# Kernel tuning notes

Hardware: AMD Instinct MI355X
Metric: run time of the kernel (lower is better)

The kernel has to match this reference:

```python
import jax, jax.numpy as jnp
import numpy as np

REGION_MAX = 116
DEFAULT_REGION_ID = 0


def setup_inputs() -> dict:
    key = jax.random.key(0)
    k1, k2, k3, k4 = jax.random.split(key, 4)
    B, N = 16, 4096
    D, H, W = 182, 218, 182
    embed_dim = 768
    # patch centers in MRI voxel space; range slightly exceeds the atlas so
    # some points land out-of-bounds and exercise the default-region path.
    patch_centers_voxels = jax.random.uniform(k1, (B, N, 3), dtype=jnp.float32) * 230.0 - 20.0
    # use identity-like affines (typical co-registered case)
    mri_affine = jnp.eye(4, dtype=jnp.float32)
    aal_affine = jnp.eye(4, dtype=jnp.float32)
    # atlas volume with integer region labels stored as float (nib get_fdata)
    aal_data = jax.random.randint(k3, (D, H, W), 0, REGION_MAX + 1).astype(jnp.float32)
    embed_table = jax.random.normal(k4, (REGION_MAX + 1, embed_dim), dtype=jnp.float32)
    return {
        "patch_centers_voxels": patch_centers_voxels,
        "mri_affine": mri_affine,
        "aal_affine": aal_affine,
        "aal_data": aal_data,
        "embed_table": embed_table,
    }


def reference(patch_centers_voxels, mri_affine, aal_affine, aal_data, embed_table):
    B, N, _ = patch_centers_voxels.shape
    D, H, W = aal_data.shape
    # homogeneous voxel coords -> world coords -> atlas voxel coords
    ones = jnp.ones((B, N, 1), dtype=patch_centers_voxels.dtype)
    voxel_homo = jnp.concatenate([patch_centers_voxels, ones], axis=-1)  # [B,N,4]
    world = jnp.einsum('ij,bnj->bni', mri_affine, voxel_homo)
    inv_aal = jnp.linalg.inv(aal_affine)
    aal_vox = jnp.einsum('ij,bnj->bni', inv_aal, world)[..., :3]  # [B,N,3]
    idx = jnp.round(aal_vox).astype(jnp.int32)  # [B,N,3]
    x, y, z = idx[..., 0], idx[..., 1], idx[..., 2]
    in_bounds = (
        (x >= 0) & (x < D) & (y >= 0) & (y < H) & (z >= 0) & (z < W)
    )
    cx = jnp.clip(x, 0, D - 1)
    cy = jnp.clip(y, 0, H - 1)
    cz = jnp.clip(z, 0, W - 1)
    region = aal_data[cx, cy, cz].astype(jnp.int32)  # [B,N]
    valid = in_bounds & (region >= 0) & (region <= REGION_MAX)
    region_ids = jnp.where(valid, region, DEFAULT_REGION_ID)
    return embed_table[region_ids]  # [B,N,embed_dim]
```

## Files before the change

kernel.cpp:

```cpp
#include <hip/hip_runtime.h>
#include <math.h>

#define REGION_MAX 116
#define EMB 768
#define EMB4 192
#define DIM_D 182
#define DIM_H 218
#define DIM_W 182

typedef float v4f __attribute__((ext_vector_type(4)));

__global__ __launch_bounds__(256) void region_kernel(
    const float* __restrict__ centers,
    const float* __restrict__ mri,
    const float* __restrict__ aal,
    const float* __restrict__ vol,
    int* __restrict__ rid_out,
    int P) {
    __shared__ float M[12];
    if (threadIdx.x == 0) {
        float a[4][8];
        for (int i = 0; i < 4; ++i)
            for (int j = 0; j < 4; ++j) {
                a[i][j]     = aal[i * 4 + j];
                a[i][j + 4] = (i == j) ? 1.0f : 0.0f;
            }
        for (int c = 0; c < 4; ++c) {
            int piv = c;
            float best = fabsf(a[c][c]);
            for (int r = c + 1; r < 4; ++r) {
                float v = fabsf(a[r][c]);
                if (v > best) { best = v; piv = r; }
            }
            if (piv != c)
                for (int j = 0; j < 8; ++j) {
                    float t = a[c][j]; a[c][j] = a[piv][j]; a[piv][j] = t;
                }
            float inv = 1.0f / a[c][c];
            for (int j = 0; j < 8; ++j) a[c][j] *= inv;
            for (int r = 0; r < 4; ++r) {
                if (r == c) continue;
                float f = a[r][c];
                for (int j = 0; j < 8; ++j) a[r][j] -= f * a[c][j];
            }
        }
        for (int i = 0; i < 3; ++i)
            for (int j = 0; j < 4; ++j) {
                float s = 0.0f;
                for (int k = 0; k < 4; ++k) s += a[i][4 + k] * mri[k * 4 + j];
                M[i * 4 + j] = s;
            }
    }
    __syncthreads();

    int p = blockIdx.x * blockDim.x + threadIdx.x;
    if (p >= P) return;

    float px = centers[p * 3 + 0];
    float py = centers[p * 3 + 1];
    float pz = centers[p * 3 + 2];

    float fx = M[0] * px + M[1] * py + M[2]  * pz + M[3];
    float fy = M[4] * px + M[5] * py + M[6]  * pz + M[7];
    float fz = M[8] * px + M[9] * py + M[10] * pz + M[11];

    int x = (int)rintf(fx);
    int y = (int)rintf(fy);
    int z = (int)rintf(fz);

    bool inb = (x >= 0) & (x < DIM_D) & (y >= 0) & (y < DIM_H) &
               (z >= 0) & (z < DIM_W);
    int cx = min(max(x, 0), DIM_D - 1);
    int cy = min(max(y, 0), DIM_H - 1);
    int cz = min(max(z, 0), DIM_W - 1);

    int region = (int)vol[((size_t)cx * DIM_H + cy) * DIM_W + cz];
    rid_out[p] = (inb && region >= 0 && region <= REGION_MAX) ? region : 0;
}

__global__ __launch_bounds__(256) void copy_kernel(
    const int* __restrict__ rid,
    const float* __restrict__ table,
    float* __restrict__ out,
    long total4) {
    long i = (long)blockIdx.x * blockDim.x + threadIdx.x;
    if (i >= total4) return;
    long p = i / EMB4;
    int  c = (int)(i - p * EMB4);
    int  r = rid[p];
    const v4f* __restrict__ src = (const v4f*)(table) + (long)r * EMB4 + c;
    v4f v = *src;
    __builtin_nontemporal_store(v, ((v4f*)out) + i);
}

extern "C" void kernel_launch(void* const* d_in, const int* in_sizes, int n_in,
                              void* d_out, int out_size, void* d_ws, size_t ws_size,
                              hipStream_t stream) {
    const float* centers = (const float*)d_in[0];
    const float* mri     = (const float*)d_in[1];
    const float* aal     = (const float*)d_in[2];
    const float* vol     = (const float*)d_in[3];
    const float* table   = (const float*)d_in[4];
    float* out = (float*)d_out;
    int*   rid = (int*)d_ws;

    int P = in_sizes[0] / 3;

    int blocks1 = (P + 255) / 256;
    region_kernel<<<blocks1, 256, 0, stream>>>(centers, mri, aal, vol, rid, P);

    long total4 = (long)P * EMB4;
    int blocks2 = (int)((total4 + 255) / 256);
    copy_kernel<<<blocks2, 256, 0, stream>>>(rid, table, out, total4);
}
```

Baseline: 227.2 us.

## Fuse region lookup and embedding gather into one kernel with shared region ids

Merges the region-index kernel and the embedding copy kernel into a single kernel. Each block handles 32 points: the first 32 threads compute region ids into shared memory, then all 256 threads stream the corresponding table rows out with nontemporal stores. This removes one launch, the workspace round trip for region ids, and the per-element 64-bit division. In exchange every block redoes the 4x4 matrix inverse and issues two barriers, and the id-computation phase is serialized ahead of the copy.

```diff
diff --git a/kernel.cpp b/kernel.cpp
--- a/kernel.cpp
+++ b/kernel.cpp
@@ -7,17 +7,22 @@
 #define DIM_D 182
 #define DIM_H 218
 #define DIM_W 182
+#define PPB 32
+#define BLOCK 256
 
 typedef float v4f __attribute__((ext_vector_type(4)));
 
-__global__ __launch_bounds__(256) void region_kernel(
+__global__ __launch_bounds__(BLOCK) void fused_embed_kernel(
     const float* __restrict__ centers,
     const float* __restrict__ mri,
     const float* __restrict__ aal,
     const float* __restrict__ vol,
-    int* __restrict__ rid_out,
+    const float* __restrict__ table,
+    float* __restrict__ out,
     int P) {
     __shared__ float M[12];
+    __shared__ int rids[PPB];
+
     if (threadIdx.x == 0) {
         float a[4][8];
         for (int i = 0; i < 4; ++i)
@@ -53,44 +58,57 @@
     }
     __syncthreads();
 
-    int p = blockIdx.x * blockDim.x + threadIdx.x;
-    if (p >= P) return;
+    const int base = blockIdx.x * PPB;
 
-    float px = centers[p * 3 + 0];
-    float py = centers[p * 3 + 1];
-    float pz = centers[p * 3 + 2];
+    if (threadIdx.x < PPB) {
+        const int p = base + threadIdx.x;
+        int r = 0;
+        if (p < P) {
+            float px = centers[p * 3 + 0];
+            float py = centers[p * 3 + 1];
+            float pz = centers[p * 3 + 2];
 
-    float fx = M[0] * px + M[1] * py + M[2]  * pz + M[3];
-    float fy = M[4] * px + M[5] * py + M[6]  * pz + M[7];
-    float fz = M[8] * px + M[9] * py + M[10] * pz + M[11];
+            float fx = M[0] * px + M[1] * py + M[2]  * pz + M[3];
+            float fy = M[4] * px + M[5] * py + M[6]  * pz + M[7];
+            float fz = M[8] * px + M[9] * py + M[10] * pz + M[11];
 
-    int x = (int)rintf(fx);
-    int y = (int)rintf(fy);
-    int z = (int)rintf(fz);
+            int x = (int)rintf(fx);
+            int y = (int)rintf(fy);
+            int z = (int)rintf(fz);
 
-    bool inb = (x >= 0) & (x < DIM_D) & (y >= 0) & (y < DIM_H) &
-               (z >= 0) & (z < DIM_W);
-    int cx = min(max(x, 0), DIM_D - 1);
-    int cy = min(max(y, 0), DIM_H - 1);
-    int cz = min(max(z, 0), DIM_W - 1);
+            bool inb = (x >= 0) & (x < DIM_D) & (y >= 0) & (y < DIM_H) &
+                       (z >= 0) & (z < DIM_W);
+            int cx = min(max(x, 0), DIM_D - 1);
+            int cy = min(max(y, 0), DIM_H - 1);
+            int cz = min(max(z, 0), DIM_W - 1);
 
-    int region = (int)vol[((size_t)cx * DIM_H + cy) * DIM_W + cz];
-    rid_out[p] = (inb && region >= 0 && region <= REGION_MAX) ? region : 0;
-}
+            int region = (int)vol[((size_t)cx * DIM_H + cy) * DIM_W + cz];
+            r = (inb && region >= 0 && region <= REGION_MAX) ? region : 0;
+        }
+        rids[threadIdx.x] = r;
+    }
+    __syncthreads();
 
-__global__ __launch_bounds__(256) void copy_kernel(
-    const int* __restrict__ rid,
-    const float* __restrict__ table,
-    float* __restrict__ out,
-    long total4) {
-    long i = (long)blockIdx.x * blockDim.x + threadIdx.x;
-    if (i >= total4) return;
-    long p = i / EMB4;
-    int  c = (int)(i - p * EMB4);
-    int  r = rid[p];
-    const v4f* __restrict__ src = (const v4f*)(table) + (long)r * EMB4 + c;
-    v4f v = *src;
-    __builtin_nontemporal_store(v, ((v4f*)out) + i);
+    const int npts = min(PPB, P - base);
+    const v4f* __restrict__ tab4 = (const v4f*)table;
+    v4f* __restrict__ out4 = (v4f*)out + (long)base * EMB4;
+
+    if (npts == PPB) {
+        #pragma unroll 4
+        for (unsigned j = threadIdx.x; j < (unsigned)(PPB * EMB4); j += BLOCK) {
+            unsigned p = j / (unsigned)EMB4;
+            unsigned c = j - p * (unsigned)EMB4;
+            v4f v = tab4[(unsigned)rids[p] * EMB4 + c];
+            __builtin_nontemporal_store(v, out4 + j);
+        }
+    } else {
+        for (unsigned j = threadIdx.x; j < (unsigned)(npts * EMB4); j += BLOCK) {
+            unsigned p = j / (unsigned)EMB4;
+            unsigned c = j - p * (unsigned)EMB4;
+            v4f v = tab4[(unsigned)rids[p] * EMB4 + c];
+            __builtin_nontemporal_store(v, out4 + j);
+        }
+    }
 }
 
 extern "C" void kernel_launch(void* const* d_in, const int* in_sizes, int n_in,
@@ -102,14 +120,9 @@
     const float* vol     = (const float*)d_in[3];
     const float* table   = (const float*)d_in[4];
     float* out = (float*)d_out;
-    int*   rid = (int*)d_ws;
 
     int P = in_sizes[0] / 3;
-
-    int blocks1 = (P + 255) / 256;
-    region_kernel<<<blocks1, 256, 0, stream>>>(centers, mri, aal, vol, rid, P);
-
-    long total4 = (long)P * EMB4;
-    int blocks2 = (int)((total4 + 255) / 256);
-    copy_kernel<<<blocks2, 256, 0, stream>>>(rid, table, out, total4);
+    int blocks = (P + PPB - 1) / PPB;
+    fused_embed_kernel<<<blocks, BLOCK, 0, stream>>>(
+        centers, mri, aal, vol, table, out, P);
 }
```

Result: slower. 232.1 us (+2.1%).
